# Optimization experiments

Hardware: AMD Instinct MI355X
Metric: run time of the kernel (lower is better)

Reference implementation:

```python
import jax, jax.numpy as jnp
import numpy as np

VOCAB, E = 100000, 128
B, S = 256, 512

def setup_inputs() -> dict:
    key = jax.random.key(0)
    k1, k2, k3, k4, k5, k6 = jax.random.split(key, 6)
    x = jax.random.randint(k1, (B, S), 0, VOCAB, dtype=jnp.int64 if jax.config.jax_enable_x64 else jnp.int32)
    emb = jax.random.normal(k2, (VOCAB, E), dtype=jnp.float32) * 0.02
    Wq = jax.random.normal(k3, (E, 1), dtype=jnp.float32) * (1.0 / np.sqrt(E))
    bq = jax.random.normal(k4, (1,), dtype=jnp.float32) * 0.01
    Wm = jax.random.normal(k5, (E, 2), dtype=jnp.float32) * (1.0 / np.sqrt(E))
    bm = jax.random.normal(k6, (2,), dtype=jnp.float32) * 0.01
    return {"x": x, "emb": emb, "Wq": Wq, "bq": bq, "Wm": Wm, "bm": bm}

def reference(x, emb, Wq, bq, Wm, bm):
    embed_x = emb[x]                                  # [B,S,E] gather
    q = embed_x @ Wq + bq                             # [B,S,1] query projection
    # torch.einsum('ijk,ijk->ij') broadcasts q's size-1 k dim:
    log_p = q[..., 0] * embed_x.sum(axis=-1)          # [B,S]
    p = jax.nn.softmax(log_p, axis=1)                 # softmax over sequence
    t_hat = jnp.einsum('bs,bse->be', p, embed_x)      # attention-weighted pool [B,E]
    return jax.nn.relu(t_hat @ Wm + bm)               # [B,2]
```

## Files before the change

kernel.cpp:

```cpp
#include <hip/hip_runtime.h>
#include <math.h>

#define VOCABSZ 100000
#define EDIM 128
#define BB 256
#define SS 512
#define NWAVE 16
#define TPW (SS / NWAVE)

__global__ __launch_bounds__(NWAVE * 64)
void fused_embed_attn_kernel(const int* __restrict__ x,
                             const float* __restrict__ emb,
                             const float* __restrict__ Wq,
                             const float* __restrict__ bq,
                             const float* __restrict__ Wm,
                             const float* __restrict__ bm,
                             float* __restrict__ out)
{
    const int b    = blockIdx.x;
    const int tid  = threadIdx.x;
    const int wave = tid >> 6;
    const int lane = tid & 63;

    const float2 wq  = *reinterpret_cast<const float2*>(Wq + 2 * lane);
    const float  bq0 = bq[0];

    int idxv = 0;
    if (lane < TPW) idxv = x[b * SS + wave * TPW + lane];

    float m = -INFINITY;
    float Z = 0.0f;
    float accx = 0.0f, accy = 0.0f;

    #pragma unroll 4
    for (int t = 0; t < TPW; ++t) {
        const int idx = __shfl(idxv, t);
        const float2 e2 = *reinterpret_cast<const float2*>(
            emb + (size_t)idx * EDIM + 2 * lane);

        float q = e2.x * wq.x + e2.y * wq.y;
        float s = e2.x + e2.y;
        #pragma unroll
        for (int off = 32; off >= 1; off >>= 1) {
            q += __shfl_xor(q, off);
            s += __shfl_xor(s, off);
        }
        const float lp = (q + bq0) * s;

        const float mn    = fmaxf(m, lp);
        const float alpha = __expf(m - mn);
        const float w     = __expf(lp - mn);
        Z    = Z * alpha + w;
        accx = accx * alpha + w * e2.x;
        accy = accy * alpha + w * e2.y;
        m = mn;
    }

    __shared__ float sm[NWAVE];
    __shared__ float sz[NWAVE];
    __shared__ float sacc[NWAVE][EDIM];
    __shared__ float th[EDIM];

    sacc[wave][2 * lane]     = accx;
    sacc[wave][2 * lane + 1] = accy;
    if (lane == 0) { sm[wave] = m; sz[wave] = Z; }
    __syncthreads();

    if (tid < EDIM) {
        float M = sm[0];
        #pragma unroll
        for (int w = 1; w < NWAVE; ++w) M = fmaxf(M, sm[w]);
        float zt = 0.0f, tv = 0.0f;
        #pragma unroll
        for (int w = 0; w < NWAVE; ++w) {
            const float sc = __expf(sm[w] - M);
            zt += sz[w] * sc;
            tv += sacc[w][tid] * sc;
        }
        th[tid] = tv / zt;
    }
    __syncthreads();

    if (tid < 64) {
        const float t0 = th[2 * tid];
        const float t1 = th[2 * tid + 1];
        const float4 wm = *reinterpret_cast<const float4*>(Wm + 4 * tid);
        float c0 = t0 * wm.x + t1 * wm.z;
        float c1 = t0 * wm.y + t1 * wm.w;
        #pragma unroll
        for (int off = 32; off >= 1; off >>= 1) {
            c0 += __shfl_xor(c0, off);
            c1 += __shfl_xor(c1, off);
        }
        if (tid == 0) {
            out[b * 2 + 0] = fmaxf(c0 + bm[0], 0.0f);
            out[b * 2 + 1] = fmaxf(c1 + bm[1], 0.0f);
        }
    }
}

extern "C" void kernel_launch(void* const* d_in, const int* in_sizes, int n_in,
                              void* d_out, int out_size, void* d_ws, size_t ws_size,
                              hipStream_t stream) {
    const int*   x   = (const int*)  d_in[0];
    const float* emb = (const float*)d_in[1];
    const float* Wq  = (const float*)d_in[2];
    const float* bq  = (const float*)d_in[3];
    const float* Wm  = (const float*)d_in[4];
    const float* bm  = (const float*)d_in[5];
    float* out = (float*)d_out;

    hipLaunchKernelGGL(fused_embed_attn_kernel, dim3(BB), dim3(NWAVE * 64), 0,
                       stream, x, emb, Wq, bq, Wm, bm, out);
}
```

Before: 107.4 us.

## Split each wave into four 16-lane rows gathering 512B rows with DPP reductions

Each wave now processes four tokens at a time: every 16-lane row loads a full 128-float embedding row with two float4 loads per lane. The per-token dot-product and sum reductions use DPP row operations in place of six-step cross-lane shuffles. All eight gathers per thread are unrolled so more loads are in flight at once. The partial softmax states of the four rows are merged with shuffles before the shared-memory combine, and the final combine is folded into the 64-thread output stage to save one barrier. The costs are more registers per thread and an extra cross-row merge step.

Measured after the change: 97.24 us. -9.4%, faster.

```diff
diff --git a/kernel.cpp b/kernel.cpp
--- a/kernel.cpp
+++ b/kernel.cpp
@@ -1,14 +1,27 @@
 #include <hip/hip_runtime.h>
 #include <math.h>
 
-#define VOCABSZ 100000
 #define EDIM 128
-#define BB 256
-#define SS 512
+#define BB   256
+#define SS   512
 #define NWAVE 16
-#define TPW (SS / NWAVE)
+#define BLOCK (NWAVE * 64)
 
-__global__ __launch_bounds__(NWAVE * 64)
+template<int CTRL>
+__device__ __forceinline__ float dpp_add(float v) {
+    int r = __builtin_amdgcn_update_dpp(0, __float_as_int(v), CTRL, 0xF, 0xF, true);
+    return v + __int_as_float(r);
+}
+
+__device__ __forceinline__ float rowsum16(float v) {
+    v = dpp_add<0xB1>(v);
+    v = dpp_add<0x4E>(v);
+    v = dpp_add<0x124>(v);
+    v = dpp_add<0x128>(v);
+    return v;
+}
+
+__global__ __launch_bounds__(BLOCK)
 void fused_embed_attn_kernel(const int* __restrict__ x,
                              const float* __restrict__ emb,
                              const float* __restrict__ Wq,
@@ -21,69 +34,85 @@
     const int tid  = threadIdx.x;
     const int wave = tid >> 6;
     const int lane = tid & 63;
+    const int row  = lane >> 4;
+    const int slot = lane & 15;
+    const int d0   = slot * 8;
 
-    const float2 wq  = *reinterpret_cast<const float2*>(Wq + 2 * lane);
+    const float4 wq0 = *reinterpret_cast<const float4*>(Wq + d0);
+    const float4 wq1 = *reinterpret_cast<const float4*>(Wq + d0 + 4);
     const float  bq0 = bq[0];
 
-    int idxv = 0;
-    if (lane < TPW) idxv = x[b * SS + wave * TPW + lane];
+    const int tbase = b * SS + wave * 32 + row * 8;
+    const int4 ia = *reinterpret_cast<const int4*>(x + tbase);
+    const int4 ib = *reinterpret_cast<const int4*>(x + tbase + 4);
+    const int idx[8] = {ia.x, ia.y, ia.z, ia.w, ib.x, ib.y, ib.z, ib.w};
 
-    float m = -INFINITY;
-    float Z = 0.0f;
-    float accx = 0.0f, accy = 0.0f;
+    float m = -INFINITY, Z = 0.f;
+    float acc[8] = {0.f, 0.f, 0.f, 0.f, 0.f, 0.f, 0.f, 0.f};
 
-    #pragma unroll 4
-    for (int t = 0; t < TPW; ++t) {
-        const int idx = __shfl(idxv, t);
-        const float2 e2 = *reinterpret_cast<const float2*>(
-            emb + (size_t)idx * EDIM + 2 * lane);
+    #pragma unroll
+    for (int i = 0; i < 8; ++i) {
+        const float* rp = emb + (size_t)idx[i] * EDIM + d0;
+        const float4 e0 = *reinterpret_cast<const float4*>(rp);
+        const float4 e1 = *reinterpret_cast<const float4*>(rp + 4);
 
-        float q = e2.x * wq.x + e2.y * wq.y;
-        float s = e2.x + e2.y;
-        #pragma unroll
-        for (int off = 32; off >= 1; off >>= 1) {
-            q += __shfl_xor(q, off);
-            s += __shfl_xor(s, off);
-        }
+        float q = e0.x * wq0.x + e0.y * wq0.y + e0.z * wq0.z + e0.w * wq0.w
+                + e1.x * wq1.x + e1.y * wq1.y + e1.z * wq1.z + e1.w * wq1.w;
+        float s = e0.x + e0.y + e0.z + e0.w + e1.x + e1.y + e1.z + e1.w;
+        q = rowsum16(q);
+        s = rowsum16(s);
         const float lp = (q + bq0) * s;
 
-        const float mn    = fmaxf(m, lp);
-        const float alpha = __expf(m - mn);
-        const float w     = __expf(lp - mn);
-        Z    = Z * alpha + w;
-        accx = accx * alpha + w * e2.x;
-        accy = accy * alpha + w * e2.y;
+        const float mn = fmaxf(m, lp);
+        const float al = __expf(m - mn);
+        const float w  = __expf(lp - mn);
+        Z = Z * al + w;
+        acc[0] = acc[0] * al + w * e0.x;  acc[1] = acc[1] * al + w * e0.y;
+        acc[2] = acc[2] * al + w * e0.z;  acc[3] = acc[3] * al + w * e0.w;
+        acc[4] = acc[4] * al + w * e1.x;  acc[5] = acc[5] * al + w * e1.y;
+        acc[6] = acc[6] * al + w * e1.z;  acc[7] = acc[7] * al + w * e1.w;
         m = mn;
     }
 
+    float m1 = fmaxf(m, __shfl_xor(m, 16));
+    const float M  = fmaxf(m1, __shfl_xor(m1, 32));
+    const float sc = __expf(m - M);
+    float Zs = Z * sc;
+    Zs += __shfl_xor(Zs, 16);
+    Zs += __shfl_xor(Zs, 32);
+    #pragma unroll
+    for (int j = 0; j < 8; ++j) {
+        float a = acc[j] * sc;
+        a += __shfl_xor(a, 16);
+        a += __shfl_xor(a, 32);
+        acc[j] = a;
+    }
+
     __shared__ float sm[NWAVE];
-    __shared__ float sz[NWAVE];
+    __shared__ float szv[NWAVE];
     __shared__ float sacc[NWAVE][EDIM];
-    __shared__ float th[EDIM];
 
-    sacc[wave][2 * lane]     = accx;
-    sacc[wave][2 * lane + 1] = accy;
-    if (lane == 0) { sm[wave] = m; sz[wave] = Z; }
-    __syncthreads();
-
-    if (tid < EDIM) {
-        float M = sm[0];
-        #pragma unroll
-        for (int w = 1; w < NWAVE; ++w) M = fmaxf(M, sm[w]);
-        float zt = 0.0f, tv = 0.0f;
-        #pragma unroll
-        for (int w = 0; w < NWAVE; ++w) {
-            const float sc = __expf(sm[w] - M);
-            zt += sz[w] * sc;
-            tv += sacc[w][tid] * sc;
-        }
-        th[tid] = tv / zt;
+    if (row == 0) {
+        *reinterpret_cast<float4*>(&sacc[wave][d0])     = make_float4(acc[0], acc[1], acc[2], acc[3]);
+        *reinterpret_cast<float4*>(&sacc[wave][d0 + 4]) = make_float4(acc[4], acc[5], acc[6], acc[7]);
+        if (slot == 0) { sm[wave] = M; szv[wave] = Zs; }
     }
     __syncthreads();
 
     if (tid < 64) {
-        const float t0 = th[2 * tid];
-        const float t1 = th[2 * tid + 1];
+        float Mb = sm[0];
+        #pragma unroll
+        for (int w = 1; w < NWAVE; ++w) Mb = fmaxf(Mb, sm[w]);
+        float zt = 0.f, tv0 = 0.f, tv1 = 0.f;
+        #pragma unroll
+        for (int w = 0; w < NWAVE; ++w) {
+            const float s2 = __expf(sm[w] - Mb);
+            zt += szv[w] * s2;
+            const float2 a2 = *reinterpret_cast<const float2*>(&sacc[w][2 * tid]);
+            tv0 += a2.x * s2;
+            tv1 += a2.y * s2;
+        }
+        const float t0 = tv0 / zt, t1 = tv1 / zt;
         const float4 wm = *reinterpret_cast<const float4*>(Wm + 4 * tid);
         float c0 = t0 * wm.x + t1 * wm.z;
         float c1 = t0 * wm.y + t1 * wm.w;
@@ -93,8 +122,8 @@
             c1 += __shfl_xor(c1, off);
         }
         if (tid == 0) {
-            out[b * 2 + 0] = fmaxf(c0 + bm[0], 0.0f);
-            out[b * 2 + 1] = fmaxf(c1 + bm[1], 0.0f);
+            out[b * 2 + 0] = fmaxf(c0 + bm[0], 0.f);
+            out[b * 2 + 1] = fmaxf(c1 + bm[1], 0.f);
         }
     }
 }
@@ -110,6 +139,6 @@
     const float* bm  = (const float*)d_in[5];
     float* out = (float*)d_out;
 
-    hipLaunchKernelGGL(fused_embed_attn_kernel, dim3(BB), dim3(NWAVE * 64), 0,
+    hipLaunchKernelGGL(fused_embed_attn_kernel, dim3(BB), dim3(BLOCK), 0,
                        stream, x, emb, Wq, bq, Wm, bm, out);
 }
```

## Precompute per-vocab projection table, then softmax over gathered scalars

Applied to the files above, without the earlier changes.

The per-token scalars (query projection, row sum, and the two output-projection dots) depend only on the vocab row, so a first kernel computes them once for all 100k rows into a float4 table in workspace. The attention kernel then gathers 16 bytes per token instead of a full 512-byte embedding row, and pools through linearity of the final projection. This replaces B*S random row gathers with one streaming pass over the 51 MB table plus small gathers. It adds a second launch and changes floating-point summation order.

New measurement: 97.46 us. 9.2% less time.

```diff
diff --git a/kernel.cpp b/kernel.cpp
--- a/kernel.cpp
+++ b/kernel.cpp
@@ -1,101 +1,119 @@
 #include <hip/hip_runtime.h>
 #include <math.h>
 
-#define VOCABSZ 100000
-#define EDIM 128
-#define BB 256
-#define SS 512
-#define NWAVE 16
-#define TPW (SS / NWAVE)
+#define VOCAB 100000
+#define EDIM  128
+#define BB    256
+#define SS    512
 
-__global__ __launch_bounds__(NWAVE * 64)
-void fused_embed_attn_kernel(const int* __restrict__ x,
-                             const float* __restrict__ emb,
-                             const float* __restrict__ Wq,
-                             const float* __restrict__ bq,
-                             const float* __restrict__ Wm,
-                             const float* __restrict__ bm,
-                             float* __restrict__ out)
+template<int CTRL>
+__device__ __forceinline__ float dpp_add(float v) {
+    int r = __builtin_amdgcn_update_dpp(0, __float_as_int(v), CTRL, 0xF, 0xF, true);
+    return v + __int_as_float(r);
+}
+
+__device__ __forceinline__ float rowsum16(float v) {
+    v = dpp_add<0xB1>(v);
+    v = dpp_add<0x4E>(v);
+    v = dpp_add<0x124>(v);
+    v = dpp_add<0x128>(v);
+    return v;
+}
+
+__global__ __launch_bounds__(1024)
+void precompute_tab(const float* __restrict__ emb,
+                    const float* __restrict__ Wq,
+                    const float* __restrict__ Wm,
+                    float4* __restrict__ tab)
 {
-    const int b    = blockIdx.x;
     const int tid  = threadIdx.x;
     const int wave = tid >> 6;
     const int lane = tid & 63;
+    const int row  = lane >> 4;
+    const int slot = lane & 15;
+    const int v    = blockIdx.x * 64 + wave * 4 + row;
+    if (v >= VOCAB) return;
 
-    const float2 wq  = *reinterpret_cast<const float2*>(Wq + 2 * lane);
-    const float  bq0 = bq[0];
+    const int dA = slot * 4;
+    const int dB = 64 + slot * 4;
 
-    int idxv = 0;
-    if (lane < TPW) idxv = x[b * SS + wave * TPW + lane];
+    const float* rp = emb + (size_t)v * EDIM;
+    const float4 e0 = *reinterpret_cast<const float4*>(rp + dA);
+    const float4 e1 = *reinterpret_cast<const float4*>(rp + dB);
 
-    float m = -INFINITY;
-    float Z = 0.0f;
-    float accx = 0.0f, accy = 0.0f;
+    const float4 wq0 = *reinterpret_cast<const float4*>(Wq + dA);
+    const float4 wq1 = *reinterpret_cast<const float4*>(Wq + dB);
+    const float4 wA0 = *reinterpret_cast<const float4*>(Wm + 2 * dA);
+    const float4 wA1 = *reinterpret_cast<const float4*>(Wm + 2 * dA + 4);
+    const float4 wB0 = *reinterpret_cast<const float4*>(Wm + 2 * dB);
+    const float4 wB1 = *reinterpret_cast<const float4*>(Wm + 2 * dB + 4);
 
-    #pragma unroll 4
-    for (int t = 0; t < TPW; ++t) {
-        const int idx = __shfl(idxv, t);
-        const float2 e2 = *reinterpret_cast<const float2*>(
-            emb + (size_t)idx * EDIM + 2 * lane);
+    float q  = e0.x * wq0.x + e0.y * wq0.y + e0.z * wq0.z + e0.w * wq0.w
+             + e1.x * wq1.x + e1.y * wq1.y + e1.z * wq1.z + e1.w * wq1.w;
+    float s  = e0.x + e0.y + e0.z + e0.w + e1.x + e1.y + e1.z + e1.w;
+    float m0 = e0.x * wA0.x + e0.y * wA0.z + e0.z * wA1.x + e0.w * wA1.z
+             + e1.x * wB0.x + e1.y * wB0.z + e1.z * wB1.x + e1.w * wB1.z;
+    float m1 = e0.x * wA0.y + e0.y * wA0.w + e0.z * wA1.y + e0.w * wA1.w
+             + e1.x * wB0.y + e1.y * wB0.w + e1.z * wB1.y + e1.w * wB1.w;
 
-        float q = e2.x * wq.x + e2.y * wq.y;
-        float s = e2.x + e2.y;
-        #pragma unroll
-        for (int off = 32; off >= 1; off >>= 1) {
-            q += __shfl_xor(q, off);
-            s += __shfl_xor(s, off);
-        }
-        const float lp = (q + bq0) * s;
+    q  = rowsum16(q);
+    s  = rowsum16(s);
+    m0 = rowsum16(m0);
+    m1 = rowsum16(m1);
 
-        const float mn    = fmaxf(m, lp);
-        const float alpha = __expf(m - mn);
-        const float w     = __expf(lp - mn);
-        Z    = Z * alpha + w;
-        accx = accx * alpha + w * e2.x;
-        accy = accy * alpha + w * e2.y;
-        m = mn;
+    if (slot == 0) tab[v] = make_float4(q, s, m0, m1);
+}
+
+__global__ __launch_bounds__(SS)
+void attn_out(const int* __restrict__ x,
+              const float4* __restrict__ tab,
+              const float* __restrict__ bq,
+              const float* __restrict__ bm,
+              float* __restrict__ out)
+{
+    const int b    = blockIdx.x;
+    const int t    = threadIdx.x;
+    const int wave = t >> 6;
+    const int lane = t & 63;
+
+    const float4 ts = tab[x[b * SS + t]];
+    const float lp  = (ts.x + bq[0]) * ts.y;
+
+    float m = lp;
+    #pragma unroll
+    for (int off = 32; off >= 1; off >>= 1) m = fmaxf(m, __shfl_xor(m, off));
+
+    __shared__ float sred[8][4];
+    if (lane == 0) sred[wave][0] = m;
+    __syncthreads();
+    float M = sred[0][0];
+    #pragma unroll
+    for (int w = 1; w < 8; ++w) M = fmaxf(M, sred[w][0]);
+
+    const float wgt = __expf(lp - M);
+    float z  = wgt;
+    float a0 = wgt * ts.z;
+    float a1 = wgt * ts.w;
+    #pragma unroll
+    for (int off = 32; off >= 1; off >>= 1) {
+        z  += __shfl_xor(z,  off);
+        a0 += __shfl_xor(a0, off);
+        a1 += __shfl_xor(a1, off);
     }
-
-    __shared__ float sm[NWAVE];
-    __shared__ float sz[NWAVE];
-    __shared__ float sacc[NWAVE][EDIM];
-    __shared__ float th[EDIM];
-
-    sacc[wave][2 * lane]     = accx;
-    sacc[wave][2 * lane + 1] = accy;
-    if (lane == 0) { sm[wave] = m; sz[wave] = Z; }
+    __syncthreads();
+    if (lane == 0) { sred[wave][1] = z; sred[wave][2] = a0; sred[wave][3] = a1; }
     __syncthreads();
 
-    if (tid < EDIM) {
-        float M = sm[0];
+    if (t == 0) {
+        float Z = 0.f, A0 = 0.f, A1 = 0.f;
         #pragma unroll
-        for (int w = 1; w < NWAVE; ++w) M = fmaxf(M, sm[w]);
-        float zt = 0.0f, tv = 0.0f;
-        #pragma unroll
-        for (int w = 0; w < NWAVE; ++w) {
-            const float sc = __expf(sm[w] - M);
-            zt += sz[w] * sc;
-            tv += sacc[w][tid] * sc;
+        for (int w = 0; w < 8; ++w) {
+            Z  += sred[w][1];
+            A0 += sred[w][2];
+            A1 += sred[w][3];
         }
-        th[tid] = tv / zt;
-    }
-    __syncthreads();
-
-    if (tid < 64) {
-        const float t0 = th[2 * tid];
-        const float t1 = th[2 * tid + 1];
-        const float4 wm = *reinterpret_cast<const float4*>(Wm + 4 * tid);
-        float c0 = t0 * wm.x + t1 * wm.z;
-        float c1 = t0 * wm.y + t1 * wm.w;
-        #pragma unroll
-        for (int off = 32; off >= 1; off >>= 1) {
-            c0 += __shfl_xor(c0, off);
-            c1 += __shfl_xor(c1, off);
-        }
-        if (tid == 0) {
-            out[b * 2 + 0] = fmaxf(c0 + bm[0], 0.0f);
-            out[b * 2 + 1] = fmaxf(c1 + bm[1], 0.0f);
-        }
+        out[b * 2 + 0] = fmaxf(A0 / Z + bm[0], 0.f);
+        out[b * 2 + 1] = fmaxf(A1 / Z + bm[1], 0.f);
     }
 }
 
@@ -108,8 +126,11 @@
     const float* bq  = (const float*)d_in[3];
     const float* Wm  = (const float*)d_in[4];
     const float* bm  = (const float*)d_in[5];
-    float* out = (float*)d_out;
+    float* out  = (float*)d_out;
+    float4* tab = (float4*)d_ws;
 
-    hipLaunchKernelGGL(fused_embed_attn_kernel, dim3(BB), dim3(NWAVE * 64), 0,
-                       stream, x, emb, Wq, bq, Wm, bm, out);
+    hipLaunchKernelGGL(precompute_tab, dim3((VOCAB + 63) / 64), dim3(1024), 0,
+                       stream, emb, Wq, Wm, tab);
+    hipLaunchKernelGGL(attn_out, dim3(BB), dim3(SS), 0, stream,
+                       x, tab, bq, bm, out);
 }
```
